# Kernel tuning notes

Measured on AMD Instinct MI355X. Metric: run time of the kernel, lower is better.

The kernel has to match this reference:

```python
import math
import jax, jax.numpy as jnp
import numpy as np

EMB = 768
N_HEAD = 12
B, T = 8, 1024

def setup_inputs() -> dict:
    key = jax.random.key(0)
    ks = jax.random.split(key, 5)
    x = jax.random.normal(ks[0], (B, T, EMB), dtype=jnp.float32)
    # linear params (torch nn.Linear: y = x @ W.T + b); store as [in, out] for einsum
    s1 = 1.0 / math.sqrt(EMB)
    W_attn = jax.random.uniform(ks[1], (EMB, 3 * EMB), jnp.float32, -s1, s1)
    b_attn = jax.random.uniform(ks[2], (3 * EMB,), jnp.float32, -s1, s1)
    W_proj = jax.random.uniform(ks[3], (EMB, EMB), jnp.float32, -s1, s1)
    b_proj = jax.random.uniform(ks[4], (EMB,), jnp.float32, -s1, s1)
    return {"x": x, "W_attn": W_attn, "b_attn": b_attn, "W_proj": W_proj, "b_proj": b_proj}

def reference(x, W_attn, b_attn, W_proj, b_proj):
    Bb, Tt, C = x.shape
    hd = C // N_HEAD
    qkv = x @ W_attn + b_attn                       # [B,T,3C]
    q, k, v = jnp.split(qkv, 3, axis=-1)
    # [B,T,C] -> [B,H,T,hd]
    def to_heads(t):
        return t.reshape(Bb, Tt, N_HEAD, hd).transpose(0, 2, 1, 3)
    q, k, v = to_heads(q), to_heads(k), to_heads(v)
    scale = 1.0 / math.sqrt(hd)
    scores = jnp.einsum('bhqd,bhkd->bhqk', q, k) * scale   # [B,H,T,T]
    causal = jnp.tril(jnp.ones((Tt, Tt), dtype=bool))
    scores = jnp.where(causal[None, None], scores, jnp.float32(-jnp.inf))
    attn = jax.nn.softmax(scores, axis=-1)
    y = jnp.einsum('bhqk,bhkd->bhqd', attn, v)              # [B,H,T,hd]
    y = y.transpose(0, 2, 1, 3).reshape(Bb, Tt, C)
    return y @ W_proj + b_proj
```

## Files before the change

kernel.cpp:

```cpp
#include <hip/hip_runtime.h>
#include <hip/hip_bf16.h>

typedef __hip_bfloat16 bf16;
typedef __attribute__((ext_vector_type(8))) short  bfrag;
typedef __attribute__((ext_vector_type(4))) float  facc;
typedef __attribute__((ext_vector_type(4))) short  short4v;

#define B_   8
#define T_   1024
#define C_   768
#define H_   12
#define HD_  64
#define M_   (B_ * T_)
#define N3_  (3 * C_)

#define QSCALE_ 0.18033688011112042f
#define M2_     17.312340490667562f

__device__ __forceinline__ float fexp2(float x) { return __builtin_amdgcn_exp2f(x); }

__device__ __forceinline__ void gload_lds16(const bf16* g, bf16* l) {
    __builtin_amdgcn_global_load_lds((const __attribute__((address_space(1))) void*)g,
                                     (__attribute__((address_space(3))) void*)l, 16, 0, 0);
}
__device__ __forceinline__ short bfbits(float f) {
    bf16 b = __float2bfloat16(f);
    return *reinterpret_cast<short*>(&b);
}

#define WAIT_VM(N) asm volatile("s_waitcnt vmcnt(" #N ")" ::: "memory")

#define XBLK 6144
#define WABLK 1728
__global__ __launch_bounds__(256) void cvt_all_kernel(
        const float* __restrict__ x,  bf16* __restrict__ xb,
        const float* __restrict__ wa, bf16* __restrict__ wat,
        const float* __restrict__ wp, bf16* __restrict__ wpt) {
    const int bid = blockIdx.x, t = threadIdx.x;
    if (bid < XBLK) {
        const size_t i = ((size_t)bid * 256 + t) * 4;
        const float4 v = *(const float4*)(x + i);
        bf16* o = xb + i;
        o[0] = __float2bfloat16(v.x); o[1] = __float2bfloat16(v.y);
        o[2] = __float2bfloat16(v.z); o[3] = __float2bfloat16(v.w);
        return;
    }
    __shared__ float tile[32][33];
    const float* w; bf16* wt; int N, tI;
    if (bid < XBLK + WABLK) { w = wa; wt = wat; N = N3_; tI = bid - XBLK; }
    else                    { w = wp; wt = wpt; N = C_;  tI = bid - XBLK - WABLK; }
    const int ntn = N / 32;
    const int n0 = (tI % ntn) * 32, k0 = (tI / ntn) * 32;
    const int tx = t & 31, ty = t >> 5;
    for (int i = ty; i < 32; i += 8) tile[i][tx] = w[(size_t)(k0 + i) * N + n0 + tx];
    __syncthreads();
    for (int i = ty; i < 32; i += 8)
        wt[(size_t)(n0 + i) * C_ + k0 + tx] = __float2bfloat16(tile[tx][i]);
}


template<int NC, bool SWAPPED>
__device__ __forceinline__ void gemm_s2_core(
        const bf16* __restrict__ Ap, const bf16* __restrict__ Bp,
        const int m0, const int n0, const int kt0,
        bf16* smem, facc (&acc)[4][NC]) {
    constexpr int KD = 768, NT = 12;
    constexpr int BN  = NC * 32;
    constexpr int BSZ = BN * 64;
    constexpr int LB  = BN / 32;
    bf16* As = smem;
    bf16* Bs = smem + 2 * 8192;
    const int t = threadIdx.x, w = t >> 6, lane = t & 63;
    const int wrow = (w >> 1) * 64;
    const int wcol = (w & 1) * (NC * 16);
    const int fr = lane & 15, quad = lane >> 4;
    const int pc0 = (quad ^ (fr & 7)) * 8;
    const int pc1 = ((quad + 4) ^ (fr & 7)) * 8;
    const int srow = t >> 3;
    const int schunk = ((t & 7) ^ (srow & 7)) * 8;
    const int sdo = t * 8;

    const bf16* Ag = Ap + (size_t)(m0 + srow) * KD + schunk;
    const bf16* Bg = Bp + (size_t)(n0 + srow) * KD + schunk;

#pragma unroll
    for (int i = 0; i < 4; ++i)
#pragma unroll
        for (int c = 0; c < NC; ++c)
#pragma unroll
            for (int r = 0; r < 4; ++r) acc[i][c][r] = 0.f;

    auto stageA = [&](bf16* dst, int k0) {
        const bf16* s = Ag + k0;
        bf16* d = dst + sdo;
#pragma unroll
        for (int r = 0; r < 4; ++r)
            gload_lds16(s + (size_t)(r * 32) * KD, d + r * 2048);
    };
    auto stageB = [&](bf16* dst, int k0) {
        const bf16* s = Bg + k0;
        bf16* d = dst + sdo;
#pragma unroll
        for (int r = 0; r < LB; ++r)
            gload_lds16(s + (size_t)(r * 32) * KD, d + r * 2048);
    };

    stageA(As, kt0 * 64);
    stageB(Bs, kt0 * 64);
    __syncthreads();

    int kt = kt0;
#pragma unroll 2
    for (int s = 0; s < NT; ++s) {
        const int cb = s & 1;
        const bf16* AsC = As + cb * 8192;
        const bf16* BsC = Bs + cb * BSZ;
        const int ktn = (kt + 1 == NT) ? 0 : kt + 1;
        if (s + 1 < NT) {
            stageA(As + (cb ^ 1) * 8192, ktn * 64);
            stageB(Bs + (cb ^ 1) * BSZ,  ktn * 64);
        }
        bfrag af[4][2];
#pragma unroll
        for (int i = 0; i < 4; ++i) {
            const bf16* ar = AsC + (wrow + i * 16 + fr) * 64;
            af[i][0] = *(const bfrag*)(ar + pc0);
            af[i][1] = *(const bfrag*)(ar + pc1);
        }
#pragma unroll
        for (int c = 0; c < NC; ++c) {
            const bf16* br = BsC + (wcol + c * 16 + fr) * 64;
            bfrag b0 = *(const bfrag*)(br + pc0);
            bfrag b1 = *(const bfrag*)(br + pc1);
#pragma unroll
            for (int i = 0; i < 4; ++i) {
                if constexpr (SWAPPED) {
                    acc[i][c] = __builtin_amdgcn_mfma_f32_16x16x32_bf16(b0, af[i][0], acc[i][c], 0, 0, 0);
                    acc[i][c] = __builtin_amdgcn_mfma_f32_16x16x32_bf16(b1, af[i][1], acc[i][c], 0, 0, 0);
                } else {
                    acc[i][c] = __builtin_amdgcn_mfma_f32_16x16x32_bf16(af[i][0], b0, acc[i][c], 0, 0, 0);
                    acc[i][c] = __builtin_amdgcn_mfma_f32_16x16x32_bf16(af[i][1], b1, acc[i][c], 0, 0, 0);
                }
            }
        }
        __syncthreads();
        kt = ktn;
    }
}

__global__ __launch_bounds__(256, 3) void qkv64_kernel(
        const bf16* __restrict__ xb, const bf16* __restrict__ wat,
        const float* __restrict__ bias,
        bf16* __restrict__ Q, bf16* __restrict__ K, bf16* __restrict__ Vt) {
    extern __shared__ bf16 smem[];
    const int id = blockIdx.x;
    const int xcd = id & 7, L = id >> 3;
    const int by = xcd * 8 + (L & 7), bx = L >> 3;
    const int m0 = by * 128, n0 = bx * 64;
    const int kt0 = L % 12;
    const int which = bx / 12;

    facc acc[4][2];
    if (which < 2) gemm_s2_core<2, true >(xb, wat, m0, n0, kt0, smem, acc);
    else           gemm_s2_core<2, false>(xb, wat, m0, n0, kt0, smem, acc);

    const int t = threadIdx.x, w = t >> 6, lane = t & 63;
    const int wr = (w >> 1) * 64, wc = (w & 1) * 32;
    const int fr = lane & 15, quad = lane >> 4;
    const int bb = m0 >> 10;
    if (which < 2) {
        bf16* dst = which ? K : Q;
        const float sc = which ? 1.0f : QSCALE_;
#pragma unroll
        for (int i = 0; i < 4; ++i) {
            const int tt = (m0 & 1023) + wr + i * 16 + fr;
#pragma unroll
            for (int c = 0; c < 2; ++c) {
                const int colbase = n0 + wc + c * 16 + quad * 4;
                const int cc = colbase - which * C_;
                const int h = cc >> 6, d0 = cc & 63;
                const float4 bv = *(const float4*)(bias + colbase);
                short4v pk;
                pk[0] = bfbits((acc[i][c][0] + bv.x) * sc);
                pk[1] = bfbits((acc[i][c][1] + bv.y) * sc);
                pk[2] = bfbits((acc[i][c][2] + bv.z) * sc);
                pk[3] = bfbits((acc[i][c][3] + bv.w) * sc);
                *(short4v*)(dst + ((size_t)(bb * H_ + h) * T_ + tt) * HD_ + d0) = pk;
            }
        }
    } else {
#pragma unroll
        for (int i = 0; i < 4; ++i) {
            const int tt0 = (m0 & 1023) + wr + i * 16 + quad * 4;
#pragma unroll
            for (int c = 0; c < 2; ++c) {
                const int col = n0 + wc + c * 16 + fr;
                const int cc = col - 2 * C_;
                const int h = cc >> 6, d = cc & 63;
                const float bv = bias[col];
                short4v pk;
                pk[0] = bfbits(acc[i][c][0] + bv);
                pk[1] = bfbits(acc[i][c][1] + bv);
                pk[2] = bfbits(acc[i][c][2] + bv);
                pk[3] = bfbits(acc[i][c][3] + bv);
                *(short4v*)(Vt + ((size_t)(bb * H_ + h) * HD_ + d) * T_ + tt0) = pk;
            }
        }
    }
}

template<bool SWAPPED>
__device__ __forceinline__ void gemm_cv_core(
        const bf16* __restrict__ Ap, const bf16* __restrict__ Bp,
        const int m0, const int n0, const int kt0,
        bf16* smem, facc (&acc)[4][3]) {
    constexpr int KD = 768, NT = 12;
    bf16* As = smem;
    bf16* Bs = smem + 2 * 8192;
    const int t = threadIdx.x, w = t >> 6, lane = t & 63;
    const int wrow = (w >> 1) * 64;
    const int wcol = (w & 1) * 48;
    const int fr = lane & 15, quad = lane >> 4;
    const int pc0 = (quad ^ (fr & 7)) * 8;
    const int pc1 = ((quad + 4) ^ (fr & 7)) * 8;
    const int srow = t >> 3;
    const int schunk = ((t & 7) ^ (srow & 7)) * 8;
    const int sdo = t * 8;

    const bf16* Ag = Ap + (size_t)(m0 + srow) * KD + schunk;
    const bf16* Bg = Bp + (size_t)(n0 + srow) * KD + schunk;

#pragma unroll
    for (int i = 0; i < 4; ++i)
#pragma unroll
        for (int c = 0; c < 3; ++c)
#pragma unroll
            for (int r = 0; r < 4; ++r) acc[i][c][r] = 0.f;

    auto stageA = [&](bf16* dst, int k0) {
        const bf16* s = Ag + k0;
        bf16* d = dst + sdo;
#pragma unroll
        for (int r = 0; r < 4; ++r)
            gload_lds16(s + (size_t)(r * 32) * KD, d + r * 2048);
    };
    auto stageB = [&](bf16* dst, int k0) {
        const bf16* s = Bg + k0;
        bf16* d = dst + sdo;
#pragma unroll
        for (int r = 0; r < 3; ++r)
            gload_lds16(s + (size_t)(r * 32) * KD, d + r * 2048);
    };

    stageA(As, kt0 * 64);
    stageB(Bs, kt0 * 64);

    int kt = kt0;
#pragma unroll 2
    for (int s = 0; s < NT; ++s) {
        const int cb = s & 1;
        const bf16* AsC = As + cb * 8192;
        const bf16* BsC = Bs + cb * 6144;
        const int ktn = (kt + 1 == NT) ? 0 : kt + 1;
        if (s + 1 < NT) {
            stageA(As + (cb ^ 1) * 8192, ktn * 64);
            stageB(Bs + (cb ^ 1) * 6144, ktn * 64);
            WAIT_VM(7);
        } else {
            WAIT_VM(0);
        }
        __builtin_amdgcn_s_barrier();
        __builtin_amdgcn_sched_barrier(0);
        __builtin_amdgcn_s_setprio(1);
        bfrag af[4][2];
#pragma unroll
        for (int i = 0; i < 4; ++i) {
            const bf16* ar = AsC + (wrow + i * 16 + fr) * 64;
            af[i][0] = *(const bfrag*)(ar + pc0);
            af[i][1] = *(const bfrag*)(ar + pc1);
        }
#pragma unroll
        for (int c = 0; c < 3; ++c) {
            const bf16* br = BsC + (wcol + c * 16 + fr) * 64;
            bfrag b0 = *(const bfrag*)(br + pc0);
            bfrag b1 = *(const bfrag*)(br + pc1);
#pragma unroll
            for (int i = 0; i < 4; ++i) {
                if constexpr (SWAPPED) {
                    acc[i][c] = __builtin_amdgcn_mfma_f32_16x16x32_bf16(b0, af[i][0], acc[i][c], 0, 0, 0);
                    acc[i][c] = __builtin_amdgcn_mfma_f32_16x16x32_bf16(b1, af[i][1], acc[i][c], 0, 0, 0);
                } else {
                    acc[i][c] = __builtin_amdgcn_mfma_f32_16x16x32_bf16(af[i][0], b0, acc[i][c], 0, 0, 0);
                    acc[i][c] = __builtin_amdgcn_mfma_f32_16x16x32_bf16(af[i][1], b1, acc[i][c], 0, 0, 0);
                }
            }
        }
        __builtin_amdgcn_s_setprio(0);
        __builtin_amdgcn_sched_barrier(0);
        __builtin_amdgcn_s_barrier();
        kt = ktn;
    }
}

__global__ __launch_bounds__(256, 2) void proj_p_kernel(
        const bf16* __restrict__ y, const bf16* __restrict__ wpt,
        const float* __restrict__ bias, float* __restrict__ out) {
    extern __shared__ bf16 smem[];
    const int id = blockIdx.x;
    const int xcd = id & 7, L = id >> 3;
    const int rgrp = xcd >> 1, cgrp = xcd & 1;
    const int r_l = L & 15, c_l = L >> 4;
    const int by = rgrp * 16 + r_l, bx = cgrp * 4 + c_l;
    const int m0 = by * 128, n0 = bx * 96;
    const int kt0 = L % 12;

    facc acc[4][3];
    gemm_cv_core<true>(y, wpt, m0, n0, kt0, smem, acc);

    const int t = threadIdx.x, w = t >> 6, lane = t & 63;
    const int wr = (w >> 1) * 64, wc = (w & 1) * 48;
    const int fr = lane & 15, quad = lane >> 4;
#pragma unroll
    for (int i = 0; i < 4; ++i) {
        const int row = m0 + wr + i * 16 + fr;
#pragma unroll
        for (int c = 0; c < 3; ++c) {
            const int colbase = n0 + wc + c * 16 + quad * 4;
            const float4 bv = *(const float4*)(bias + colbase);
            float4 v;
            v.x = acc[i][c][0] + bv.x;
            v.y = acc[i][c][1] + bv.y;
            v.z = acc[i][c][2] + bv.z;
            v.w = acc[i][c][3] + bv.w;
            *(float4*)(out + (size_t)row * C_ + colbase) = v;
        }
    }
}

__global__ __launch_bounds__(256) void flash_attn_kernel(
        const bf16* __restrict__ Q, const bf16* __restrict__ K,
        const bf16* __restrict__ Vt, bf16* __restrict__ Y) {
    const int id   = blockIdx.x;
    const int bh   = (id & 7) * 12 + ((id >> 3) % 12);
    const int qpair = (id >> 3) / 12;
    const int t = threadIdx.x, w = t >> 6, lane = t & 63;
    const int fr = lane & 15, quad = lane >> 4, fq = quad * 8;

    __shared__ bf16 sK[2][64 * 64];
    __shared__ bf16 sVt[2][64 * 64];
    __shared__ bf16 sP[4][16][72];

    const bf16* Kbh = K  + (size_t)bh * T_ * HD_;
    const bf16* Vbh = Vt + (size_t)bh * HD_ * T_;
    const int b_ = bh / H_, h_ = bh % H_;

    const int srow = t >> 3;
    const int sgc  = ((t & 7) ^ (srow & 7)) * 8;
    const int c0   = (quad ^ (fr & 7)) * 8;

    for (int phase = 0; phase < 2; ++phase) {
        const int qt = (phase == 0) ? (15 - qpair) : qpair;
        const int q0 = qt * 64;

        const bf16* qbase = Q + ((size_t)bh * T_ + q0 + w * 16 + fr) * HD_;
        bfrag qa0 = *(const bfrag*)(qbase + fq);
        bfrag qa1 = *(const bfrag*)(qbase + 32 + fq);

        facc o[4];
        for (int nb = 0; nb < 4; ++nb) for (int r = 0; r < 4; ++r) o[nb][r] = 0.f;
        float rowl[4] = {0.f, 0.f, 0.f, 0.f};

        auto tile_step = [&](int kt, const bf16* sKp, const bf16* sVp) {
            const int k0 = kt * 64;
            facc s[4];
            for (int nb = 0; nb < 4; ++nb) for (int r = 0; r < 4; ++r) s[nb][r] = 0.f;
            __builtin_amdgcn_s_setprio(1);
            for (int nb = 0; nb < 4; ++nb) {
                const bf16* kr = sKp + (nb * 16 + fr) * 64;
                bfrag kb0 = *(const bfrag*)(kr + c0);
                bfrag kb1 = *(const bfrag*)(kr + (c0 ^ 32));
                s[nb] = __builtin_amdgcn_mfma_f32_16x16x32_bf16(qa0, kb0, s[nb], 0, 0, 0);
                s[nb] = __builtin_amdgcn_mfma_f32_16x16x32_bf16(qa1, kb1, s[nb], 0, 0, 0);
            }
            __builtin_amdgcn_s_setprio(0);
            const int mrow0 = q0 + w * 16 + quad * 4;
            float p[4][4];
            if (kt == qt) {
                for (int nb = 0; nb < 4; ++nb) {
                    const int n_g = k0 + nb * 16 + fr;
                    for (int r = 0; r < 4; ++r) {
                        const float a = (n_g > mrow0 + r) ? -1e30f : s[nb][r] - M2_;
                        p[nb][r] = fexp2(a);
                    }
                }
            } else {
                for (int nb = 0; nb < 4; ++nb)
                    for (int r = 0; r < 4; ++r)
                        p[nb][r] = fexp2(s[nb][r] - M2_);
            }
            for (int r = 0; r < 4; ++r)
                rowl[r] += p[0][r] + p[1][r] + p[2][r] + p[3][r];
            for (int nb = 0; nb < 4; ++nb)
                for (int r = 0; r < 4; ++r)
                    sP[w][quad * 4 + r][nb * 16 + fr] = __float2bfloat16(p[nb][r]);
            bfrag pa0 = *(const bfrag*)(&sP[w][fr][fq]);
            bfrag pa1 = *(const bfrag*)(&sP[w][fr][32 + fq]);
            __builtin_amdgcn_s_setprio(1);
            for (int nb = 0; nb < 4; ++nb) {
                const bf16* vr = sVp + (nb * 16 + fr) * 64;
                bfrag vb0 = *(const bfrag*)(vr + c0);
                bfrag vb1 = *(const bfrag*)(vr + (c0 ^ 32));
                o[nb] = __builtin_amdgcn_mfma_f32_16x16x32_bf16(pa0, vb0, o[nb], 0, 0, 0);
                o[nb] = __builtin_amdgcn_mfma_f32_16x16x32_bf16(pa1, vb1, o[nb], 0, 0, 0);
            }
            __builtin_amdgcn_s_setprio(0);
        };

        for (int kt = 0; kt <= qt; kt += 2) {
            const int k0 = kt * 64;
            const bool two = (kt + 1 <= qt);
            gload_lds16(Kbh + (size_t)(k0 + srow) * HD_ + sgc,      sK[0] + t * 8);
            gload_lds16(Kbh + (size_t)(k0 + 32 + srow) * HD_ + sgc, sK[0] + 2048 + t * 8);
            gload_lds16(Vbh + (size_t)srow * T_ + k0 + sgc,         sVt[0] + t * 8);
            gload_lds16(Vbh + (size_t)(srow + 32) * T_ + k0 + sgc,  sVt[0] + 2048 + t * 8);
            if (two) {
                const int k1 = k0 + 64;
                gload_lds16(Kbh + (size_t)(k1 + srow) * HD_ + sgc,      sK[1] + t * 8);
                gload_lds16(Kbh + (size_t)(k1 + 32 + srow) * HD_ + sgc, sK[1] + 2048 + t * 8);
                gload_lds16(Vbh + (size_t)srow * T_ + k1 + sgc,         sVt[1] + t * 8);
                gload_lds16(Vbh + (size_t)(srow + 32) * T_ + k1 + sgc,  sVt[1] + 2048 + t * 8);
            }
            __syncthreads();
            tile_step(kt, sK[0], sVt[0]);
            if (two) tile_step(kt + 1, sK[1], sVt[1]);
            __syncthreads();
        }

        for (int r = 0; r < 4; ++r) {
            float l = rowl[r];
            l += __shfl_xor(l, 1);
            l += __shfl_xor(l, 2);
            l += __shfl_xor(l, 4);
            l += __shfl_xor(l, 8);
            const float inv = 1.0f / l;
            const int tt = q0 + w * 16 + quad * 4 + r;
            bf16* yrow = Y + ((size_t)b_ * T_ + tt) * C_ + h_ * HD_;
            for (int nb = 0; nb < 4; ++nb)
                yrow[nb * 16 + fr] = __float2bfloat16(o[nb][r] * inv);
        }
    }
}

extern "C" void kernel_launch(void* const* d_in, const int* in_sizes, int n_in,
                              void* d_out, int out_size, void* d_ws, size_t ws_size,
                              hipStream_t stream) {
    const float* x      = (const float*)d_in[0];
    const float* W_attn = (const float*)d_in[1];
    const float* b_attn = (const float*)d_in[2];
    const float* W_proj = (const float*)d_in[3];
    const float* b_proj = (const float*)d_in[4];
    float* out = (float*)d_out;

    const size_t per = (size_t)B_ * H_ * T_ * HD_;
    bf16* Q   = (bf16*)d_ws;
    bf16* K   = Q + per;
    bf16* Vt  = K + per;
    bf16* XbY = Vt + per;
    bf16* WaT = XbY + per;
    bf16* WpT = WaT + (size_t)N3_ * C_;

    static bool s_attr = false;
    if (!s_attr) {
        hipFuncSetAttribute((const void*)qkv64_kernel,
                            hipFuncAttributeMaxDynamicSharedMemorySize, 49152);
        hipFuncSetAttribute((const void*)proj_p_kernel,
                            hipFuncAttributeMaxDynamicSharedMemorySize, 57344);
        s_attr = true;
    }

    cvt_all_kernel<<<dim3(XBLK + WABLK + 576), dim3(256), 0, stream>>>(
        x, XbY, W_attn, WaT, W_proj, WpT);
    qkv64_kernel<<<dim3(2304), dim3(256), 49152, stream>>>(
        XbY, WaT, b_attn, Q, K, Vt);
    flash_attn_kernel<<<dim3(768), dim3(256), 0, stream>>>(Q, K, Vt, XbY);
    proj_p_kernel<<<dim3(512), dim3(256), 57344, stream>>>(
        XbY, WpT, b_proj, out);
}
```

Before: 177.9 us.

## Share K/V tiles between paired query tiles and batch B fragment loads in GEMMs

The attention kernel now processes its high and low query tiles in a single pass over K/V. Each staged K/V tile is used by both query tiles, so the low tile no longer reloads K/V from global memory. This keeps two sets of accumulators live and raises register pressure; launch bounds now target 3 blocks per CU. The GEMM inner loops also load all B fragments up front and issue the MFMAs in two k-halves to give the scheduler more independent work.

```diff
diff --git a/kernel.cpp b/kernel.cpp
--- a/kernel.cpp
+++ b/kernel.cpp
@@ -120,7 +120,7 @@
             stageA(As + (cb ^ 1) * 8192, ktn * 64);
             stageB(Bs + (cb ^ 1) * BSZ,  ktn * 64);
         }
-        bfrag af[4][2];
+        bfrag af[4][2], bfr[NC][2];
 #pragma unroll
         for (int i = 0; i < 4; ++i) {
             const bf16* ar = AsC + (wrow + i * 16 + fr) * 64;
@@ -130,19 +130,27 @@
 #pragma unroll
         for (int c = 0; c < NC; ++c) {
             const bf16* br = BsC + (wcol + c * 16 + fr) * 64;
-            bfrag b0 = *(const bfrag*)(br + pc0);
-            bfrag b1 = *(const bfrag*)(br + pc1);
+            bfr[c][0] = *(const bfrag*)(br + pc0);
+            bfr[c][1] = *(const bfrag*)(br + pc1);
+        }
+#pragma unroll
+        for (int c = 0; c < NC; ++c)
 #pragma unroll
             for (int i = 0; i < 4; ++i) {
-                if constexpr (SWAPPED) {
-                    acc[i][c] = __builtin_amdgcn_mfma_f32_16x16x32_bf16(b0, af[i][0], acc[i][c], 0, 0, 0);
-                    acc[i][c] = __builtin_amdgcn_mfma_f32_16x16x32_bf16(b1, af[i][1], acc[i][c], 0, 0, 0);
-                } else {
-                    acc[i][c] = __builtin_amdgcn_mfma_f32_16x16x32_bf16(af[i][0], b0, acc[i][c], 0, 0, 0);
-                    acc[i][c] = __builtin_amdgcn_mfma_f32_16x16x32_bf16(af[i][1], b1, acc[i][c], 0, 0, 0);
-                }
-            }
-        }
+                if constexpr (SWAPPED)
+                    acc[i][c] = __builtin_amdgcn_mfma_f32_16x16x32_bf16(bfr[c][0], af[i][0], acc[i][c], 0, 0, 0);
+                else
+                    acc[i][c] = __builtin_amdgcn_mfma_f32_16x16x32_bf16(af[i][0], bfr[c][0], acc[i][c], 0, 0, 0);
+            }
+#pragma unroll
+        for (int c = 0; c < NC; ++c)
+#pragma unroll
+            for (int i = 0; i < 4; ++i) {
+                if constexpr (SWAPPED)
+                    acc[i][c] = __builtin_amdgcn_mfma_f32_16x16x32_bf16(bfr[c][1], af[i][1], acc[i][c], 0, 0, 0);
+                else
+                    acc[i][c] = __builtin_amdgcn_mfma_f32_16x16x32_bf16(af[i][1], bfr[c][1], acc[i][c], 0, 0, 0);
+            }
         __syncthreads();
         kt = ktn;
     }
@@ -272,7 +280,7 @@
         __builtin_amdgcn_s_barrier();
         __builtin_amdgcn_sched_barrier(0);
         __builtin_amdgcn_s_setprio(1);
-        bfrag af[4][2];
+        bfrag af[4][2], bfr[3][2];
 #pragma unroll
         for (int i = 0; i < 4; ++i) {
             const bf16* ar = AsC + (wrow + i * 16 + fr) * 64;
@@ -282,19 +290,27 @@
 #pragma unroll
         for (int c = 0; c < 3; ++c) {
             const bf16* br = BsC + (wcol + c * 16 + fr) * 64;
-            bfrag b0 = *(const bfrag*)(br + pc0);
-            bfrag b1 = *(const bfrag*)(br + pc1);
+            bfr[c][0] = *(const bfrag*)(br + pc0);
+            bfr[c][1] = *(const bfrag*)(br + pc1);
+        }
+#pragma unroll
+        for (int c = 0; c < 3; ++c)
 #pragma unroll
             for (int i = 0; i < 4; ++i) {
-                if constexpr (SWAPPED) {
-                    acc[i][c] = __builtin_amdgcn_mfma_f32_16x16x32_bf16(b0, af[i][0], acc[i][c], 0, 0, 0);
-                    acc[i][c] = __builtin_amdgcn_mfma_f32_16x16x32_bf16(b1, af[i][1], acc[i][c], 0, 0, 0);
-                } else {
-                    acc[i][c] = __builtin_amdgcn_mfma_f32_16x16x32_bf16(af[i][0], b0, acc[i][c], 0, 0, 0);
-                    acc[i][c] = __builtin_amdgcn_mfma_f32_16x16x32_bf16(af[i][1], b1, acc[i][c], 0, 0, 0);
-                }
-            }
-        }
+                if constexpr (SWAPPED)
+                    acc[i][c] = __builtin_amdgcn_mfma_f32_16x16x32_bf16(bfr[c][0], af[i][0], acc[i][c], 0, 0, 0);
+                else
+                    acc[i][c] = __builtin_amdgcn_mfma_f32_16x16x32_bf16(af[i][0], bfr[c][0], acc[i][c], 0, 0, 0);
+            }
+#pragma unroll
+        for (int c = 0; c < 3; ++c)
+#pragma unroll
+            for (int i = 0; i < 4; ++i) {
+                if constexpr (SWAPPED)
+                    acc[i][c] = __builtin_amdgcn_mfma_f32_16x16x32_bf16(bfr[c][1], af[i][1], acc[i][c], 0, 0, 0);
+                else
+                    acc[i][c] = __builtin_amdgcn_mfma_f32_16x16x32_bf16(af[i][1], bfr[c][1], acc[i][c], 0, 0, 0);
+            }
         __builtin_amdgcn_s_setprio(0);
         __builtin_amdgcn_sched_barrier(0);
         __builtin_amdgcn_s_barrier();
@@ -337,7 +353,7 @@
     }
 }
 
-__global__ __launch_bounds__(256) void flash_attn_kernel(
+__global__ __launch_bounds__(256, 3) void flash_attn_kernel(
         const bf16* __restrict__ Q, const bf16* __restrict__ K,
         const bf16* __restrict__ Vt, bf16* __restrict__ Y) {
     const int id   = blockIdx.x;
@@ -358,84 +374,101 @@
     const int sgc  = ((t & 7) ^ (srow & 7)) * 8;
     const int c0   = (quad ^ (fr & 7)) * 8;
 
-    for (int phase = 0; phase < 2; ++phase) {
-        const int qt = (phase == 0) ? (15 - qpair) : qpair;
-        const int q0 = qt * 64;
-
-        const bf16* qbase = Q + ((size_t)bh * T_ + q0 + w * 16 + fr) * HD_;
-        bfrag qa0 = *(const bfrag*)(qbase + fq);
-        bfrag qa1 = *(const bfrag*)(qbase + 32 + fq);
-
-        facc o[4];
-        for (int nb = 0; nb < 4; ++nb) for (int r = 0; r < 4; ++r) o[nb][r] = 0.f;
-        float rowl[4] = {0.f, 0.f, 0.f, 0.f};
-
-        auto tile_step = [&](int kt, const bf16* sKp, const bf16* sVp) {
-            const int k0 = kt * 64;
-            facc s[4];
-            for (int nb = 0; nb < 4; ++nb) for (int r = 0; r < 4; ++r) s[nb][r] = 0.f;
-            __builtin_amdgcn_s_setprio(1);
+    const int qtH = 15 - qpair, qtL = qpair;
+    const int q0H = qtH * 64,  q0L = qtL * 64;
+
+    const bf16* qbH = Q + ((size_t)bh * T_ + q0H + w * 16 + fr) * HD_;
+    const bf16* qbL = Q + ((size_t)bh * T_ + q0L + w * 16 + fr) * HD_;
+    bfrag qaH0 = *(const bfrag*)(qbH + fq);
+    bfrag qaH1 = *(const bfrag*)(qbH + 32 + fq);
+    bfrag qaL0 = *(const bfrag*)(qbL + fq);
+    bfrag qaL1 = *(const bfrag*)(qbL + 32 + fq);
+
+    facc oH[4], oL[4];
+    float rlH[4] = {0.f, 0.f, 0.f, 0.f}, rlL[4] = {0.f, 0.f, 0.f, 0.f};
+    for (int nb = 0; nb < 4; ++nb)
+        for (int r = 0; r < 4; ++r) { oH[nb][r] = 0.f; oL[nb][r] = 0.f; }
+
+    auto tile_step = [&](int kt, int qt, int q0,
+                         const bfrag& qa0, const bfrag& qa1,
+                         facc (&o)[4], float (&rowl)[4],
+                         const bf16* sKp, const bf16* sVp) {
+        const int k0 = kt * 64;
+        facc s[4];
+        for (int nb = 0; nb < 4; ++nb) for (int r = 0; r < 4; ++r) s[nb][r] = 0.f;
+        __builtin_amdgcn_s_setprio(1);
+        for (int nb = 0; nb < 4; ++nb) {
+            const bf16* kr = sKp + (nb * 16 + fr) * 64;
+            bfrag kb0 = *(const bfrag*)(kr + c0);
+            bfrag kb1 = *(const bfrag*)(kr + (c0 ^ 32));
+            s[nb] = __builtin_amdgcn_mfma_f32_16x16x32_bf16(qa0, kb0, s[nb], 0, 0, 0);
+            s[nb] = __builtin_amdgcn_mfma_f32_16x16x32_bf16(qa1, kb1, s[nb], 0, 0, 0);
+        }
+        __builtin_amdgcn_s_setprio(0);
+        const int mrow0 = q0 + w * 16 + quad * 4;
+        float p[4][4];
+        if (kt == qt) {
             for (int nb = 0; nb < 4; ++nb) {
-                const bf16* kr = sKp + (nb * 16 + fr) * 64;
-                bfrag kb0 = *(const bfrag*)(kr + c0);
-                bfrag kb1 = *(const bfrag*)(kr + (c0 ^ 32));
-                s[nb] = __builtin_amdgcn_mfma_f32_16x16x32_bf16(qa0, kb0, s[nb], 0, 0, 0);
-                s[nb] = __builtin_amdgcn_mfma_f32_16x16x32_bf16(qa1, kb1, s[nb], 0, 0, 0);
-            }
-            __builtin_amdgcn_s_setprio(0);
-            const int mrow0 = q0 + w * 16 + quad * 4;
-            float p[4][4];
-            if (kt == qt) {
-                for (int nb = 0; nb < 4; ++nb) {
-                    const int n_g = k0 + nb * 16 + fr;
-                    for (int r = 0; r < 4; ++r) {
-                        const float a = (n_g > mrow0 + r) ? -1e30f : s[nb][r] - M2_;
-                        p[nb][r] = fexp2(a);
-                    }
+                const int n_g = k0 + nb * 16 + fr;
+                for (int r = 0; r < 4; ++r) {
+                    const float a = (n_g > mrow0 + r) ? -1e30f : s[nb][r] - M2_;
+                    p[nb][r] = fexp2(a);
                 }
-            } else {
-                for (int nb = 0; nb < 4; ++nb)
-                    for (int r = 0; r < 4; ++r)
-                        p[nb][r] = fexp2(s[nb][r] - M2_);
-            }
-            for (int r = 0; r < 4; ++r)
-                rowl[r] += p[0][r] + p[1][r] + p[2][r] + p[3][r];
+            }
+        } else {
             for (int nb = 0; nb < 4; ++nb)
                 for (int r = 0; r < 4; ++r)
-                    sP[w][quad * 4 + r][nb * 16 + fr] = __float2bfloat16(p[nb][r]);
-            bfrag pa0 = *(const bfrag*)(&sP[w][fr][fq]);
-            bfrag pa1 = *(const bfrag*)(&sP[w][fr][32 + fq]);
-            __builtin_amdgcn_s_setprio(1);
-            for (int nb = 0; nb < 4; ++nb) {
-                const bf16* vr = sVp + (nb * 16 + fr) * 64;
-                bfrag vb0 = *(const bfrag*)(vr + c0);
-                bfrag vb1 = *(const bfrag*)(vr + (c0 ^ 32));
-                o[nb] = __builtin_amdgcn_mfma_f32_16x16x32_bf16(pa0, vb0, o[nb], 0, 0, 0);
-                o[nb] = __builtin_amdgcn_mfma_f32_16x16x32_bf16(pa1, vb1, o[nb], 0, 0, 0);
-            }
-            __builtin_amdgcn_s_setprio(0);
-        };
-
-        for (int kt = 0; kt <= qt; kt += 2) {
-            const int k0 = kt * 64;
-            const bool two = (kt + 1 <= qt);
-            gload_lds16(Kbh + (size_t)(k0 + srow) * HD_ + sgc,      sK[0] + t * 8);
-            gload_lds16(Kbh + (size_t)(k0 + 32 + srow) * HD_ + sgc, sK[0] + 2048 + t * 8);
-            gload_lds16(Vbh + (size_t)srow * T_ + k0 + sgc,         sVt[0] + t * 8);
-            gload_lds16(Vbh + (size_t)(srow + 32) * T_ + k0 + sgc,  sVt[0] + 2048 + t * 8);
-            if (two) {
-                const int k1 = k0 + 64;
-                gload_lds16(Kbh + (size_t)(k1 + srow) * HD_ + sgc,      sK[1] + t * 8);
-                gload_lds16(Kbh + (size_t)(k1 + 32 + srow) * HD_ + sgc, sK[1] + 2048 + t * 8);
-                gload_lds16(Vbh + (size_t)srow * T_ + k1 + sgc,         sVt[1] + t * 8);
-                gload_lds16(Vbh + (size_t)(srow + 32) * T_ + k1 + sgc,  sVt[1] + 2048 + t * 8);
-            }
-            __syncthreads();
-            tile_step(kt, sK[0], sVt[0]);
-            if (two) tile_step(kt + 1, sK[1], sVt[1]);
-            __syncthreads();
-        }
-
+                    p[nb][r] = fexp2(s[nb][r] - M2_);
+        }
+        for (int r = 0; r < 4; ++r)
+            rowl[r] += p[0][r] + p[1][r] + p[2][r] + p[3][r];
+        for (int nb = 0; nb < 4; ++nb)
+            for (int r = 0; r < 4; ++r)
+                sP[w][quad * 4 + r][nb * 16 + fr] = __float2bfloat16(p[nb][r]);
+        bfrag pa0 = *(const bfrag*)(&sP[w][fr][fq]);
+        bfrag pa1 = *(const bfrag*)(&sP[w][fr][32 + fq]);
+        __builtin_amdgcn_s_setprio(1);
+        for (int nb = 0; nb < 4; ++nb) {
+            const bf16* vr = sVp + (nb * 16 + fr) * 64;
+            bfrag vb0 = *(const bfrag*)(vr + c0);
+            bfrag vb1 = *(const bfrag*)(vr + (c0 ^ 32));
+            o[nb] = __builtin_amdgcn_mfma_f32_16x16x32_bf16(pa0, vb0, o[nb], 0, 0, 0);
+            o[nb] = __builtin_amdgcn_mfma_f32_16x16x32_bf16(pa1, vb1, o[nb], 0, 0, 0);
+        }
+        __builtin_amdgcn_s_setprio(0);
+    };
+
+    for (int kt = 0; kt <= qtH; kt += 2) {
+        const int k0 = kt * 64;
+        const bool two = (kt + 1 <= qtH);
+        gload_lds16(Kbh + (size_t)(k0 + srow) * HD_ + sgc,      sK[0] + t * 8);
+        gload_lds16(Kbh + (size_t)(k0 + 32 + srow) * HD_ + sgc, sK[0] + 2048 + t * 8);
+        gload_lds16(Vbh + (size_t)srow * T_ + k0 + sgc,         sVt[0] + t * 8);
+        gload_lds16(Vbh + (size_t)(srow + 32) * T_ + k0 + sgc,  sVt[0] + 2048 + t * 8);
+        if (two) {
+            const int k1 = k0 + 64;
+            gload_lds16(Kbh + (size_t)(k1 + srow) * HD_ + sgc,      sK[1] + t * 8);
+            gload_lds16(Kbh + (size_t)(k1 + 32 + srow) * HD_ + sgc, sK[1] + 2048 + t * 8);
+            gload_lds16(Vbh + (size_t)srow * T_ + k1 + sgc,         sVt[1] + t * 8);
+            gload_lds16(Vbh + (size_t)(srow + 32) * T_ + k1 + sgc,  sVt[1] + 2048 + t * 8);
+        }
+        __syncthreads();
+        tile_step(kt, qtH, q0H, qaH0, qaH1, oH, rlH, sK[0], sVt[0]);
+        if (kt <= qtL)
+            tile_step(kt, qtL, q0L, qaL0, qaL1, oL, rlL, sK[0], sVt[0]);
+        if (two) {
+            tile_step(kt + 1, qtH, q0H, qaH0, qaH1, oH, rlH, sK[1], sVt[1]);
+            if (kt + 1 <= qtL)
+                tile_step(kt + 1, qtL, q0L, qaL0, qaL1, oL, rlL, sK[1], sVt[1]);
+        }
+        __syncthreads();
+    }
+
+#pragma unroll
+    for (int e = 0; e < 2; ++e) {
+        facc* o = e ? oL : oH;
+        float* rowl = e ? rlL : rlH;
+        const int q0 = e ? q0L : q0H;
         for (int r = 0; r < 4; ++r) {
             float l = rowl[r];
             l += __shfl_xor(l, 1);
```

Measured after the change: 176.1 us. About the same (-1.0%).
